# Kernel tuning notes

Hardware: AMD Instinct MI355X
Metric: run time of the kernel (lower is better)

Reference implementation:

```python
import jax, jax.numpy as jnp
import numpy as np

MUL0, MUL1 = 32, 16          # multiplicities of 0e and 1o in irreps_node
RBF, HID = 16, 64
O1 = MUL0 * MUL0             # path 0e x 0e -> 0e
O2 = O1 + MUL0 * MUL1        # path 0e x 1o -> 1o
O3 = O2 + MUL1 * MUL1        # path 1o x 0e -> 1o
WNUMEL = O3 + MUL1 * MUL0    # path 1o x 1o -> 0e  => 2304 total
C_PATH = 1.0 / np.sqrt(MUL0 + MUL1).astype(np.float32)  # per-output fan-in norm
C_110 = 1.0 / np.sqrt(3.0)   # CG factor for 1o x 1o -> 0e (component norm)


def setup_inputs() -> dict:
    key = jax.random.key(0)
    ks = jax.random.split(key, 16)
    N, E = 50000, 200000
    x = jax.random.normal(ks[0], (N, MUL0 + 3 * MUL1), jnp.float32)
    edge_src = jax.random.randint(ks[1], (E,), 0, N)
    edge_dst = jax.random.randint(ks[2], (E,), 0, N)
    edge_sh = jax.random.normal(ks[3], (E, 4), jnp.float32)
    edge_rbf = jax.random.uniform(ks[4], (E, RBF), jnp.float32)
    # RadialMLP params (fan-in scaled init)
    w1 = jax.random.normal(ks[5], (RBF, HID), jnp.float32) / np.sqrt(RBF)
    b1 = jnp.zeros((HID,), jnp.float32)
    w2 = jax.random.normal(ks[6], (HID, HID), jnp.float32) / np.sqrt(HID)
    b2 = jnp.zeros((HID,), jnp.float32)
    w3 = jax.random.normal(ks[7], (HID, WNUMEL), jnp.float32) / np.sqrt(HID)
    b3 = jnp.zeros((WNUMEL,), jnp.float32)
    # o3.Linear weights (per-irrep mixing, fan-in normalization folded in)
    ws_self = jax.random.normal(ks[8], (MUL0, MUL0), jnp.float32) / np.sqrt(MUL0)
    wv_self = jax.random.normal(ks[9], (MUL1, MUL1), jnp.float32) / np.sqrt(MUL1)
    ws_out = jax.random.normal(ks[10], (MUL0, MUL0), jnp.float32) / np.sqrt(MUL0)
    wv_out = jax.random.normal(ks[11], (MUL1, MUL1), jnp.float32) / np.sqrt(MUL1)
    return {"x": x, "edge_src": edge_src, "edge_dst": edge_dst,
            "edge_sh": edge_sh, "edge_rbf": edge_rbf,
            "w1": w1, "b1": b1, "w2": w2, "b2": b2, "w3": w3, "b3": b3,
            "ws_self": ws_self, "wv_self": wv_self,
            "ws_out": ws_out, "wv_out": wv_out}


def _irrep_linear(x, ws, wv):
    # per-irrep mixing of '32x0e + 16x1o' features; x: [N, 80]
    n = x.shape[0]
    s = x[:, :MUL0] @ ws                                     # [N, 32]
    v = jnp.einsum('nid,io->nod', x[:, MUL0:].reshape(n, MUL1, 3), wv)
    return jnp.concatenate([s, v.reshape(n, 3 * MUL1)], axis=-1)


def reference(x, edge_src, edge_dst, edge_sh, edge_rbf,
              w1, b1, w2, b2, w3, b3, ws_self, wv_self, ws_out, wv_out):
    N = x.shape[0]
    E = edge_rbf.shape[0]
    # radial MLP -> per-edge TP weights [E, 2304]
    h = jax.nn.silu(edge_rbf @ w1 + b1)
    h = jax.nn.silu(h @ w2 + b2)
    W = h @ w3 + b3
    W1 = W[:, :O1].reshape(E, MUL0, MUL0)      # 0e x 0e -> 0e
    W2 = W[:, O1:O2].reshape(E, MUL0, MUL1)    # 0e x 1o -> 1o
    W3 = W[:, O2:O3].reshape(E, MUL1, MUL1)    # 1o x 0e -> 1o
    W4 = W[:, O3:].reshape(E, MUL1, MUL0)      # 1o x 1o -> 0e
    # gather source node features per edge
    xs = x[edge_src, :MUL0]                                   # [E, 32]
    xv = x[edge_src, MUL0:].reshape(E, MUL1, 3)               # [E, 16, 3]
    sh_s = edge_sh[:, 0]                                      # [E]
    sh_v = edge_sh[:, 1:4]                                    # [E, 3]
    # CG tensor product paths
    out_s = jnp.einsum('ei,eio->eo', xs * sh_s[:, None], W1)
    out_s = out_s + C_110 * jnp.einsum('eid,ed,eio->eo', xv, sh_v, W4)
    out_v = jnp.einsum('ei,ed,eio->eod', xs, sh_v, W2)
    out_v = out_v + jnp.einsum('eid,eio->eod', xv * sh_s[:, None, None], W3)
    m = C_PATH * jnp.concatenate([out_s, out_v.reshape(E, 3 * MUL1)], axis=-1)
    # scatter-add + degree normalize
    agg = jax.ops.segment_sum(m, edge_dst, num_segments=N)
    deg = jax.ops.segment_sum(jnp.ones((E,), x.dtype), edge_dst, num_segments=N)
    agg = agg / jnp.maximum(deg, 1.0)[:, None]
    return _irrep_linear(x, ws_self, wv_self) + _irrep_linear(agg, ws_out, wv_out)
```

## Files before the change

### kernel.cpp

```cpp
#include <hip/hip_runtime.h>
#include <math.h>

#define MUL0    32
#define MUL1    16
#define RBFD    16
#define HIDD    64
#define WNUMEL  2304
#define FDIM    80
#define CPATH   0.14433756729740643f
#define C110    0.57735026918962576f

#define TE       128
#define NTHREADS 512
#define NITER    48

#define W3N_ELEMS (NITER*6*512)
#define W1B_ELEMS (4*64*8)
#define W2B_ELEMS (4*2*64*8)

#define FS4_U16  0
#define XS_U16   2048
#define XV_U16   6144
#define SH_B     24576
#define SRC_B    26624
#define DST_B    27136
#define B3_B     27648
#define SMEM_B   36864

typedef float          f32x4   __attribute__((ext_vector_type(4)));
typedef short          short8  __attribute__((ext_vector_type(8)));
typedef short          short4v __attribute__((ext_vector_type(4)));
typedef unsigned short u16;

__device__ __forceinline__ float silu(float v) {
    return v / (1.0f + __expf(-v));
}
__device__ __forceinline__ u16 f2bf(float f) {
    unsigned int u = __float_as_uint(f);
    u += 0x7fffu + ((u >> 16) & 1u);
    return (u16)(u >> 16);
}
__device__ __forceinline__ float bf2f(u16 s) {
    return __uint_as_float(((unsigned int)s) << 16);
}
__device__ __forceinline__ f32x4 cvt4(short4v s) {
    f32x4 r;
    r[0] = bf2f((u16)s[0]); r[1] = bf2f((u16)s[1]);
    r[2] = bf2f((u16)s[2]); r[3] = bf2f((u16)s[3]);
    return r;
}
__device__ __forceinline__ f32x4 mfma16(short8 a, short8 b, f32x4 c) {
    return __builtin_amdgcn_mfma_f32_16x16x32_bf16(a, b, c, 0, 0, 0);
}

__device__ __forceinline__ int tile_of(int t, int pair) {
    if (t < 32) return (pair == 0) ? 2*t : (pair == 1) ? 2*t + 1 : 64 + t;
    int tt = t - 32;
    return (pair == 0) ? 112 + 2*tt : (pair == 1) ? 113 + 2*tt : 96 + tt;
}

__global__ void k_prep(const float* __restrict__ w3,
                       const float* __restrict__ w1,
                       const float* __restrict__ w2,
                       u16* __restrict__ w3n,
                       u16* __restrict__ w1b,
                       u16* __restrict__ w2b) {
    int idx = blockIdx.x * 256 + threadIdx.x;
    if (idx < W3N_ELEMS) {
        int j = idx & 7, l = (idx >> 3) & 63, f = idx >> 9;
        int t = f / 6, s = f - 6 * t, pair = s >> 1, kh = s & 1;
        int tile = tile_of(t, pair);
        int k = kh * 32 + 8 * (l >> 4) + j;
        int c = tile * 16 + (l & 15);
        w3n[idx] = f2bf(CPATH * w3[k * WNUMEL + c]);
        return;
    }
    idx -= W3N_ELEMS;
    if (idx < W1B_ELEMS) {
        int j = idx & 7, l = (idx >> 3) & 63, ct = idx >> 9;
        int k = 8 * (l >> 4) + j;
        int c = ct * 16 + (l & 15);
        w1b[idx] = (k < RBFD) ? f2bf(w1[k * HIDD + c]) : (u16)0;
        return;
    }
    idx -= W1B_ELEMS;
    if (idx < W2B_ELEMS) {
        int j = idx & 7, l = (idx >> 3) & 63, kh = (idx >> 9) & 1, ct = idx >> 10;
        int k = kh * 32 + 8 * (l >> 4) + j;
        int c = ct * 16 + (l & 15);
        w2b[idx] = f2bf(w2[k * HIDD + c]);
    }
}

#define COMPUTE(T, BP) do {                                                    \
    float bs0 = s_b3[(T)*48 + lo];                                             \
    float bs1 = s_b3[(T)*48 + 16 + lo];                                        \
    float bs2 = s_b3[(T)*48 + 32 + lo];                                        \
    f32x4 tA = {bs0,bs0,bs0,bs0};                                              \
    tA = mfma16(a0, BP[0], tA); tA = mfma16(a1, BP[1], tA);                    \
    f32x4 tB = {bs1,bs1,bs1,bs1};                                              \
    tB = mfma16(a0, BP[2], tB); tB = mfma16(a1, BP[3], tB);                    \
    f32x4 tC = {bs2,bs2,bs2,bs2};                                              \
    tC = mfma16(a0, BP[4], tC); tC = mfma16(a1, BP[5], tC);                    \
    if ((T) < 32) {                                                            \
        f32x4 fx = cvt4(*(const short4v*)&S[XS_U16 + w*512 + (T)*16 + 4*g]);   \
        f32x4 f1 = fx * sh0v;                                                  \
        acc[0] += f1 * tA;                                                     \
        acc[1] += f1 * tB;                                                     \
        acc[2] += fx * tC;                                                     \
    } else {                                                                   \
        const int i_ = (T) - 32;                                               \
        f32x4 f4 = cvt4(*(const short4v*)&S[FS4_U16 + w*256 + i_*16 + 4*g]);   \
        acc[0] += f4 * tA;                                                     \
        acc[1] += f4 * tB;                                                     \
        acc[3] += cvt4(*(const short4v*)&S[XV_U16 + w*768 + (0 +i_)*16 + 4*g]) * tC; \
        acc[4] += cvt4(*(const short4v*)&S[XV_U16 + w*768 + (16+i_)*16 + 4*g]) * tC; \
        acc[5] += cvt4(*(const short4v*)&S[XV_U16 + w*768 + (32+i_)*16 + 4*g]) * tC; \
    }                                                                          \
} while (0)

__global__ __launch_bounds__(NTHREADS, 4)
void k_edge(const float* __restrict__ x,
            const int*   __restrict__ esrc,
            const int*   __restrict__ edst,
            const float* __restrict__ esh,
            const float* __restrict__ erbf,
            const u16*   __restrict__ w1b,
            const float* __restrict__ b1,
            const u16*   __restrict__ w2b,
            const float* __restrict__ b2,
            const u16*   __restrict__ w3n,
            const float* __restrict__ b3,
            float* __restrict__ agg,
            float* __restrict__ deg,
            int E)
{
    __shared__ alignas(16) unsigned char smem[SMEM_B];
    u16*   S     = (u16*)smem;
    float* s_sh  = (float*)(smem + SH_B);
    int*   s_src = (int*)(smem + SRC_B);
    int*   s_dst = (int*)(smem + DST_B);
    float* s_b3  = (float*)(smem + B3_B);

    const int tid = threadIdx.x;
    const int eb  = blockIdx.x * TE;
    const int w   = tid >> 6;
    const int l   = tid & 63;
    const int lo  = l & 15;
    const int g   = l >> 4;

    if (tid < TE) {
        int eg = eb + tid;
        s_src[tid] = (eg < E) ? esrc[eg] : 0;
        s_dst[tid] = (eg < E) ? edst[eg] : 0;
    }
    {
        long eg4 = (long)eb * 4 + tid;
        s_sh[tid] = (eg4 < (long)E * 4) ? esh[eg4] : 0.0f;
    }
    __syncthreads();

    float cb1[4], cb2[4];
    #pragma unroll
    for (int ct = 0; ct < 4; ++ct) { cb1[ct] = b1[ct*16 + lo]; cb2[ct] = b2[ct*16 + lo]; }
    const short8* W1B = (const short8*)w1b;
    const short8* W2B = (const short8*)w2b;
    const int e0 = 16 * w;

    {
        short8 ar = {0,0,0,0,0,0,0,0};
        if (g < 2 && (eb + e0 + lo) < E) {
            const float* rp = erbf + (size_t)(eb + e0 + lo) * RBFD + 8 * g;
            f32x4 r0 = *(const f32x4*)rp;
            f32x4 r1 = *(const f32x4*)(rp + 4);
            ar[0]=f2bf(r0[0]); ar[1]=f2bf(r0[1]); ar[2]=f2bf(r0[2]); ar[3]=f2bf(r0[3]);
            ar[4]=f2bf(r1[0]); ar[5]=f2bf(r1[1]); ar[6]=f2bf(r1[2]); ar[7]=f2bf(r1[3]);
        }
        #pragma unroll
        for (int ct = 0; ct < 4; ++ct) {
            f32x4 t = {cb1[ct], cb1[ct], cb1[ct], cb1[ct]};
            t = mfma16(ar, W1B[ct * 64 + l], t);
            #pragma unroll
            for (int r = 0; r < 4; ++r)
                S[(e0 + 4*g + r) * 72 + ct*16 + lo] = f2bf(silu(t[r]));
        }
    }
    {
        short8 h0 = *(const short8*)&S[(e0 + lo) * 72 + 0  + 8*g];
        short8 h1 = *(const short8*)&S[(e0 + lo) * 72 + 32 + 8*g];
        #pragma unroll
        for (int ct = 0; ct < 4; ++ct) {
            f32x4 t = {cb2[ct], cb2[ct], cb2[ct], cb2[ct]};
            t = mfma16(h0, W2B[(ct*2 + 0) * 64 + l], t);
            t = mfma16(h1, W2B[(ct*2 + 1) * 64 + l], t);
            #pragma unroll
            for (int r = 0; r < 4; ++r)
                S[(e0 + 4*g + r) * 72 + ct*16 + lo] = f2bf(silu(t[r]));
        }
    }
    short8 a0 = *(const short8*)&S[(e0 + lo) * 72 + 0  + 8*g];
    short8 a1 = *(const short8*)&S[(e0 + lo) * 72 + 32 + 8*g];
    __syncthreads();

    if (tid < TE) {
        const int el = tid, grp = el >> 4, e16 = el & 15;
        const float sh0 = s_sh[el*4 + 0];
        const float sh1 = s_sh[el*4 + 1];
        const float sh2 = s_sh[el*4 + 2];
        const float sh3 = s_sh[el*4 + 3];
        const float* xrow = x + (size_t)s_src[el] * FDIM;
        u16* fs4B = S + FS4_U16 + grp * 256 + e16;
        u16* xsB  = S + XS_U16  + grp * 512 + e16;
        u16* xvB  = S + XV_U16  + grp * 768 + e16;
        #pragma unroll
        for (int v = 0; v < 8; ++v) {
            f32x4 x4 = *(const f32x4*)(xrow + 4 * v);
            #pragma unroll
            for (int c2 = 0; c2 < 4; ++c2)
                xsB[(4 * v + c2) * 16] = f2bf(x4[c2]);
        }
        float buf[48];
        #pragma unroll
        for (int v = 0; v < 12; ++v) {
            f32x4 t4 = *(const f32x4*)(xrow + MUL0 + 4 * v);
            buf[4*v]=t4[0]; buf[4*v+1]=t4[1]; buf[4*v+2]=t4[2]; buf[4*v+3]=t4[3];
        }
        #pragma unroll
        for (int i = 0; i < 16; ++i) {
            float v0 = buf[3*i], v1 = buf[3*i+1], v2 = buf[3*i+2];
            xvB[(0  + i) * 16] = f2bf(v0 * sh0);
            xvB[(16 + i) * 16] = f2bf(v1 * sh0);
            xvB[(32 + i) * 16] = f2bf(v2 * sh0);
            fs4B[i * 16]       = f2bf(C110 * (v0*sh1 + v1*sh2 + v2*sh3));
        }
    } else {
        for (int idx = tid - TE; idx < WNUMEL; idx += NTHREADS - TE) {
            int t = idx / 48, r = idx - 48 * t, pair = r >> 4, lo16 = r & 15;
            s_b3[idx] = CPATH * b3[tile_of(t, pair) * 16 + lo16];
        }
    }
    __syncthreads();

    f32x4 sh0v;
    #pragma unroll
    for (int r = 0; r < 4; ++r)
        sh0v[r] = s_sh[(16*w + 4*g + r) * 4];

    const short8* WB = (const short8*)w3n;
    f32x4 acc[6];
    #pragma unroll
    for (int p = 0; p < 6; ++p) acc[p] = (f32x4){0.f,0.f,0.f,0.f};

    short8 p0[6], p1[6], p2[6];
    #pragma unroll
    for (int s = 0; s < 6; ++s) {
        p0[s] = WB[0*384 + s*64 + l];
        p1[s] = WB[1*384 + s*64 + l];
        p2[s] = WB[2*384 + s*64 + l];
    }

    for (int t = 0; t < NITER; t += 3) {
        COMPUTE(t, p0);
        {   const int tn = (t + 3 < NITER) ? (t + 3) : 0;
            #pragma unroll
            for (int s = 0; s < 6; ++s) p0[s] = WB[tn*384 + s*64 + l];
        }
        COMPUTE(t + 1, p1);
        {   const int tn = (t + 4 < NITER) ? (t + 4) : 0;
            #pragma unroll
            for (int s = 0; s < 6; ++s) p1[s] = WB[tn*384 + s*64 + l];
        }
        COMPUTE(t + 2, p2);
        {   const int tn = (t + 5 < NITER) ? (t + 5) : 0;
            #pragma unroll
            for (int s = 0; s < 6; ++s) p2[s] = WB[tn*384 + s*64 + l];
        }
    }

    #pragma unroll
    for (int r = 0; r < 4; ++r) {
        const int e_loc = 16*w + 4*g + r;
        float* row = agg + (size_t)s_dst[e_loc] * FDIM;
        float sv0 = s_sh[e_loc*4 + 1];
        float sv1 = s_sh[e_loc*4 + 2];
        float sv2 = s_sh[e_loc*4 + 3];
        atomicAdd(row + lo,      acc[0][r]);
        atomicAdd(row + 16 + lo, acc[1][r]);
        atomicAdd(row + MUL0 + lo*3 + 0, sv0*acc[2][r] + acc[3][r]);
        atomicAdd(row + MUL0 + lo*3 + 1, sv1*acc[2][r] + acc[4][r]);
        atomicAdd(row + MUL0 + lo*3 + 2, sv2*acc[2][r] + acc[5][r]);
    }
    if (tid < TE && (eb + tid) < E) atomicAdd(deg + s_dst[tid], 1.0f);
}

#define NPB 16
__global__ __launch_bounds__(256)
void k_node(const float* __restrict__ x,
            const float* __restrict__ deg,
            const float* __restrict__ ws_self,
            const float* __restrict__ wv_self,
            const float* __restrict__ ws_out,
            const float* __restrict__ wv_out,
            float* __restrict__ out)
{
    __shared__ float s_x[NPB][81];
    __shared__ float s_a[NPB][81];
    __shared__ float s_inv[NPB];

    const int tid = threadIdx.x;
    const int n0  = blockIdx.x * NPB;

    if (tid < NPB) s_inv[tid] = 1.0f / fmaxf(deg[n0 + tid], 1.0f);
    const float* xb = x   + (size_t)n0 * FDIM;
    const float* ab = out + (size_t)n0 * FDIM;
    for (int idx = tid; idx < NPB * FDIM; idx += 256) {
        int nl = idx / FDIM, jj = idx - nl * FDIM;
        s_x[nl][jj] = xb[idx];
        s_a[nl][jj] = ab[idx];
    }
    __syncthreads();

    const int j  = tid & 15;
    const int nl = tid >> 4;
    const float inv = s_inv[nl];
    float* orow = out + (size_t)(n0 + nl) * FDIM;

    float s1s = 0.f, s1a = 0.f, s2s = 0.f, s2a = 0.f;
    #pragma unroll
    for (int i = 0; i < MUL0; ++i) {
        float xs = s_x[nl][i], as = s_a[nl][i];
        s1s += xs * ws_self[i * MUL0 + j];
        s1a += as * ws_out [i * MUL0 + j];
        s2s += xs * ws_self[i * MUL0 + j + 16];
        s2a += as * ws_out [i * MUL0 + j + 16];
    }
    orow[j]      = s1s + inv * s1a;
    orow[j + 16] = s2s + inv * s2a;

    float vs[3] = {0.f,0.f,0.f}, va[3] = {0.f,0.f,0.f};
    #pragma unroll
    for (int i = 0; i < MUL1; ++i) {
        float wsf = wv_self[i * MUL1 + j];
        float wof = wv_out [i * MUL1 + j];
        #pragma unroll
        for (int d = 0; d < 3; ++d) {
            vs[d] += s_x[nl][MUL0 + 3*i + d] * wsf;
            va[d] += s_a[nl][MUL0 + 3*i + d] * wof;
        }
    }
    #pragma unroll
    for (int d = 0; d < 3; ++d)
        orow[MUL0 + j*3 + d] = vs[d] + inv * va[d];
}

extern "C" void kernel_launch(void* const* d_in, const int* in_sizes, int n_in,
                              void* d_out, int out_size, void* d_ws, size_t ws_size,
                              hipStream_t stream)
{
    const float* x       = (const float*)d_in[0];
    const int*   esrc    = (const int*)  d_in[1];
    const int*   edst    = (const int*)  d_in[2];
    const float* esh     = (const float*)d_in[3];
    const float* erbf    = (const float*)d_in[4];
    const float* w1      = (const float*)d_in[5];
    const float* b1      = (const float*)d_in[6];
    const float* w2      = (const float*)d_in[7];
    const float* b2      = (const float*)d_in[8];
    const float* w3      = (const float*)d_in[9];
    const float* b3      = (const float*)d_in[10];
    const float* ws_self = (const float*)d_in[11];
    const float* wv_self = (const float*)d_in[12];
    const float* ws_out  = (const float*)d_in[13];
    const float* wv_out  = (const float*)d_in[14];

    const int N = in_sizes[0] / FDIM;
    const int E = in_sizes[1];

    char* wsp = (char*)d_ws;
    float* deg = (float*)wsp;
    size_t off = ((size_t)N * sizeof(float) + 255) & ~(size_t)255;
    u16* w3n = (u16*)(wsp + off);
    off += ((size_t)W3N_ELEMS * 2 + 255) & ~(size_t)255;
    u16* w1b = (u16*)(wsp + off);
    off += ((size_t)W1B_ELEMS * 2 + 255) & ~(size_t)255;
    u16* w2b = (u16*)(wsp + off);

    hipMemsetAsync(d_out, 0, (size_t)out_size * sizeof(float), stream);
    hipMemsetAsync(deg, 0, (size_t)N * sizeof(float), stream);

    k_prep<<<(W3N_ELEMS + W1B_ELEMS + W2B_ELEMS + 255) / 256, 256, 0, stream>>>(
        w3, w1, w2, w3n, w1b, w2b);

    const int nblk = (E + TE - 1) / TE;
    k_edge<<<nblk, NTHREADS, 0, stream>>>(
        x, esrc, edst, esh, erbf, w1b, b1, w2b, b2, w3n, b3,
        (float*)d_out, deg, E);

    k_node<<<N / NPB, 256, 0, stream>>>(
        x, deg, ws_self, wv_self, ws_out, wv_out, (float*)d_out);
}
```

Baseline: 245.4 us.

## Sort edges by destination and merge same-destination atomics per lane

```diff
diff --git a/kernel.cpp b/kernel.cpp
--- a/kernel.cpp
+++ b/kernel.cpp
@@ -25,7 +25,8 @@
 #define SRC_B    26624
 #define DST_B    27136
 #define B3_B     27648
-#define SMEM_B   36864
+#define EID_B    36864
+#define SMEM_B   37376
 
 typedef float          f32x4   __attribute__((ext_vector_type(4)));
 typedef short          short8  __attribute__((ext_vector_type(8)));
@@ -89,6 +90,48 @@
         int k = kh * 32 + 8 * (l >> 4) + j;
         int c = ct * 16 + (l & 15);
         w2b[idx] = f2bf(w2[k * HIDD + c]);
+    }
+}
+
+__global__ void k_cnt(const int* __restrict__ edst, int* __restrict__ cnt, int E) {
+    int e = blockIdx.x * 256 + threadIdx.x;
+    if (e < E) atomicAdd(&cnt[edst[e]], 1);
+}
+
+__global__ __launch_bounds__(1024)
+void k_scan(const int* __restrict__ cnt, int* __restrict__ base, int N) {
+    __shared__ int part[1024];
+    const int t = threadIdx.x;
+    const int chunk = (N + 1023) / 1024;
+    int s = 0;
+    for (int k = 0; k < chunk; ++k) {
+        int i = t * chunk + k;
+        if (i < N) s += cnt[i];
+    }
+    part[t] = s;
+    __syncthreads();
+    for (int off = 1; off < 1024; off <<= 1) {
+        int v = (t >= off) ? part[t - off] : 0;
+        __syncthreads();
+        part[t] += v;
+        __syncthreads();
+    }
+    int run = part[t] - s;
+    for (int k = 0; k < chunk; ++k) {
+        int i = t * chunk + k;
+        if (i < N) { base[i] = run; run += cnt[i]; }
+    }
+}
+
+__global__ void k_fill(const int* __restrict__ edst,
+                       const int* __restrict__ base,
+                       int* __restrict__ cursor,
+                       int* __restrict__ eidx, int E) {
+    int e = blockIdx.x * 256 + threadIdx.x;
+    if (e < E) {
+        int d = edst[e];
+        int p = atomicAdd(&cursor[d], 1);
+        eidx[base[d] + p] = e;
     }
 }
 
@@ -125,6 +168,7 @@
             const int*   __restrict__ edst,
             const float* __restrict__ esh,
             const float* __restrict__ erbf,
+            const int*   __restrict__ eidx,
             const u16*   __restrict__ w1b,
             const float* __restrict__ b1,
             const u16*   __restrict__ w2b,
@@ -132,7 +176,6 @@
             const u16*   __restrict__ w3n,
             const float* __restrict__ b3,
             float* __restrict__ agg,
-            float* __restrict__ deg,
             int E)
 {
     __shared__ alignas(16) unsigned char smem[SMEM_B];
@@ -141,6 +184,7 @@
     int*   s_src = (int*)(smem + SRC_B);
     int*   s_dst = (int*)(smem + DST_B);
     float* s_b3  = (float*)(smem + B3_B);
+    int*   s_eid = (int*)(smem + EID_B);
 
     const int tid = threadIdx.x;
     const int eb  = blockIdx.x * TE;
@@ -150,13 +194,14 @@
     const int g   = l >> 4;
 
     if (tid < TE) {
-        int eg = eb + tid;
-        s_src[tid] = (eg < E) ? esrc[eg] : 0;
-        s_dst[tid] = (eg < E) ? edst[eg] : 0;
-    }
-    {
-        long eg4 = (long)eb * 4 + tid;
-        s_sh[tid] = (eg4 < (long)E * 4) ? esh[eg4] : 0.0f;
+        int eg  = eb + tid;
+        int eid = (eg < E) ? eidx[eg] : 0;
+        s_eid[tid] = eid;
+        s_src[tid] = esrc[eid];
+        s_dst[tid] = (eg < E) ? edst[eid] : 0;
+        f32x4 sh4 = {0.f, 0.f, 0.f, 0.f};
+        if (eg < E) sh4 = *(const f32x4*)(esh + (size_t)eid * 4);
+        *(f32x4*)&s_sh[tid * 4] = sh4;
     }
     __syncthreads();
 
@@ -170,7 +215,7 @@
     {
         short8 ar = {0,0,0,0,0,0,0,0};
         if (g < 2 && (eb + e0 + lo) < E) {
-            const float* rp = erbf + (size_t)(eb + e0 + lo) * RBFD + 8 * g;
+            const float* rp = erbf + (size_t)s_eid[e0 + lo] * RBFD + 8 * g;
             f32x4 r0 = *(const f32x4*)rp;
             f32x4 r1 = *(const f32x4*)(rp + 4);
             ar[0]=f2bf(r0[0]); ar[1]=f2bf(r0[1]); ar[2]=f2bf(r0[2]); ar[3]=f2bf(r0[3]);
@@ -277,26 +322,42 @@
         }
     }
 
+    int   dl[4];
+    float o0[4], o1[4], o2[4], o3[4], o4[4];
     #pragma unroll
     for (int r = 0; r < 4; ++r) {
         const int e_loc = 16*w + 4*g + r;
-        float* row = agg + (size_t)s_dst[e_loc] * FDIM;
+        dl[r] = s_dst[e_loc];
         float sv0 = s_sh[e_loc*4 + 1];
         float sv1 = s_sh[e_loc*4 + 2];
         float sv2 = s_sh[e_loc*4 + 3];
-        atomicAdd(row + lo,      acc[0][r]);
-        atomicAdd(row + 16 + lo, acc[1][r]);
-        atomicAdd(row + MUL0 + lo*3 + 0, sv0*acc[2][r] + acc[3][r]);
-        atomicAdd(row + MUL0 + lo*3 + 1, sv1*acc[2][r] + acc[4][r]);
-        atomicAdd(row + MUL0 + lo*3 + 2, sv2*acc[2][r] + acc[5][r]);
-    }
-    if (tid < TE && (eb + tid) < E) atomicAdd(deg + s_dst[tid], 1.0f);
+        o0[r] = acc[0][r];
+        o1[r] = acc[1][r];
+        o2[r] = sv0*acc[2][r] + acc[3][r];
+        o3[r] = sv1*acc[2][r] + acc[4][r];
+        o4[r] = sv2*acc[2][r] + acc[5][r];
+    }
+    float c0 = 0.f, c1 = 0.f, c2 = 0.f, c3 = 0.f, c4 = 0.f;
+    #pragma unroll
+    for (int r = 0; r < 4; ++r) {
+        c0 += o0[r]; c1 += o1[r]; c2 += o2[r]; c3 += o3[r]; c4 += o4[r];
+        bool flush = (r == 3) || (dl[r + 1] != dl[r]);
+        if (flush) {
+            float* row = agg + (size_t)dl[r] * FDIM;
+            atomicAdd(row + lo,      c0);
+            atomicAdd(row + 16 + lo, c1);
+            atomicAdd(row + MUL0 + lo*3 + 0, c2);
+            atomicAdd(row + MUL0 + lo*3 + 1, c3);
+            atomicAdd(row + MUL0 + lo*3 + 2, c4);
+            c0 = c1 = c2 = c3 = c4 = 0.f;
+        }
+    }
 }
 
 #define NPB 16
 __global__ __launch_bounds__(256)
 void k_node(const float* __restrict__ x,
-            const float* __restrict__ deg,
+            const int*   __restrict__ cnt,
             const float* __restrict__ ws_self,
             const float* __restrict__ wv_self,
             const float* __restrict__ ws_out,
@@ -310,7 +371,7 @@
     const int tid = threadIdx.x;
     const int n0  = blockIdx.x * NPB;
 
-    if (tid < NPB) s_inv[tid] = 1.0f / fmaxf(deg[n0 + tid], 1.0f);
+    if (tid < NPB) s_inv[tid] = 1.0f / fmaxf((float)cnt[n0 + tid], 1.0f);
     const float* xb = x   + (size_t)n0 * FDIM;
     const float* ab = out + (size_t)n0 * FDIM;
     for (int idx = tid; idx < NPB * FDIM; idx += 256) {
@@ -377,25 +438,36 @@
     const int E = in_sizes[1];
 
     char* wsp = (char*)d_ws;
-    float* deg = (float*)wsp;
-    size_t off = ((size_t)N * sizeof(float) + 255) & ~(size_t)255;
-    u16* w3n = (u16*)(wsp + off);
-    off += ((size_t)W3N_ELEMS * 2 + 255) & ~(size_t)255;
-    u16* w1b = (u16*)(wsp + off);
-    off += ((size_t)W1B_ELEMS * 2 + 255) & ~(size_t)255;
-    u16* w2b = (u16*)(wsp + off);
+    size_t off = 0;
+    auto take = [&](size_t bytes) {
+        char* p = wsp + off;
+        off += (bytes + 255) & ~(size_t)255;
+        return p;
+    };
+    int* cnt    = (int*)take((size_t)N * 4);
+    int* base   = (int*)take((size_t)N * 4);
+    int* cursor = (int*)take((size_t)N * 4);
+    int* eidx   = (int*)take((size_t)E * 4);
+    u16* w3n    = (u16*)take((size_t)W3N_ELEMS * 2);
+    u16* w1b    = (u16*)take((size_t)W1B_ELEMS * 2);
+    u16* w2b    = (u16*)take((size_t)W2B_ELEMS * 2);
 
     hipMemsetAsync(d_out, 0, (size_t)out_size * sizeof(float), stream);
-    hipMemsetAsync(deg, 0, (size_t)N * sizeof(float), stream);
+    hipMemsetAsync(cnt, 0, (size_t)N * 4, stream);
+    hipMemsetAsync(cursor, 0, (size_t)N * 4, stream);
 
     k_prep<<<(W3N_ELEMS + W1B_ELEMS + W2B_ELEMS + 255) / 256, 256, 0, stream>>>(
         w3, w1, w2, w3n, w1b, w2b);
 
+    k_cnt <<<(E + 255) / 256, 256, 0, stream>>>(edst, cnt, E);
+    k_scan<<<1, 1024, 0, stream>>>(cnt, base, N);
+    k_fill<<<(E + 255) / 256, 256, 0, stream>>>(edst, base, cursor, eidx, E);
+
     const int nblk = (E + TE - 1) / TE;
     k_edge<<<nblk, NTHREADS, 0, stream>>>(
-        x, esrc, edst, esh, erbf, w1b, b1, w2b, b2, w3n, b3,
-        (float*)d_out, deg, E);
+        x, esrc, edst, esh, erbf, eidx, w1b, b1, w2b, b2, w3n, b3,
+        (float*)d_out, E);
 
     k_node<<<N / NPB, 256, 0, stream>>>(
-        x, deg, ws_self, wv_self, ws_out, wv_out, (float*)d_out);
-}
+        x, cnt, ws_self, wv_self, ws_out, wv_out, (float*)d_out);
+}
```

Result: slower. 316.7 us (+29.0%).
